# Kernel tuning notes

Measured on AMD Instinct MI355X. Metric: run time of the kernel, lower is better.

## Reference

```python
import jax, jax.numpy as jnp
import numpy as np

N_NODES = 50000
D_FEAT = 128
HIDDEN = 256
CLASSES = 40
N_EDGES = 800000


def setup_inputs() -> dict:
    key = jax.random.key(0)
    ks = jax.random.split(key, 8)
    x = jax.random.normal(ks[0], (N_NODES, D_FEAT), dtype=jnp.float32)
    edge_index = jax.random.randint(ks[1], (2, N_EDGES), 0, N_NODES, dtype=jnp.int64)
    s1 = 1.0 / np.sqrt(D_FEAT)
    s2 = 1.0 / np.sqrt(HIDDEN)
    # PyG SAGEConv: lin_l (applied to aggregated neighbors, has bias), lin_r (root, no bias)
    Wl1 = jax.random.uniform(ks[2], (HIDDEN, D_FEAT), jnp.float32, -s1, s1)
    bl1 = jnp.zeros((HIDDEN,), jnp.float32)
    Wr1 = jax.random.uniform(ks[3], (HIDDEN, D_FEAT), jnp.float32, -s1, s1)
    Wl2 = jax.random.uniform(ks[4], (CLASSES, HIDDEN), jnp.float32, -s2, s2)
    bl2 = jnp.zeros((CLASSES,), jnp.float32)
    Wr2 = jax.random.uniform(ks[5], (CLASSES, HIDDEN), jnp.float32, -s2, s2)
    return {"x": x, "edge_index": edge_index, "Wl1": Wl1, "bl1": bl1, "Wr1": Wr1,
            "Wl2": Wl2, "bl2": bl2, "Wr2": Wr2}


def _mean_aggregate(x, src, dst, n_nodes):
    # gather source features along edges, scatter-mean into destinations
    summed = jax.ops.segment_sum(x[src], dst, num_segments=n_nodes)  # [N, d]
    counts = jax.ops.segment_sum(jnp.ones((src.shape[0],), x.dtype), dst,
                                 num_segments=n_nodes)
    return summed / jnp.maximum(counts, 1.0)[:, None]


def _sage_conv(x, src, dst, Wl, bl, Wr):
    agg = _mean_aggregate(x, src, dst, x.shape[0])
    return agg @ Wl.T + bl + x @ Wr.T


def reference(x, edge_index, Wl1, bl1, Wr1, Wl2, bl2, Wr2):
    src, dst = edge_index[0], edge_index[1]
    h = _sage_conv(x, src, dst, Wl1, bl1, Wr1)
    h = jax.nn.relu(h)
    # F.dropout(training=self.training): eval-mode inference -> identity
    h = _sage_conv(h, src, dst, Wl2, bl2, Wr2)
    return jax.nn.log_softmax(h, axis=1)
```

## Files before the change

### kernel.cpp

```cpp
#include <hip/hip_runtime.h>
#include <hip/hip_bf16.h>
#include <math.h>

#define N_NODES 50000
#define D_FEAT  128
#define HIDDEN  256
#define CLASSES 40
#define N_EDGES 800000
#define R2S 48
#define HLS 264
#define ALS 136
#define NTILES 3125
#define GRID_L 512
#define NBUCK 196
#define BCAP  5120
#define BA_BLOCKS 784
#define WCVT_BLOCKS 336

typedef unsigned int  u32;
typedef unsigned short u16;
typedef __attribute__((ext_vector_type(8))) short short8;
typedef __attribute__((ext_vector_type(4))) float floatx4;

__device__ __forceinline__ float bf_lo(u32 w) { union { u32 i; float f; } u; u.i = w << 16; return u.f; }
__device__ __forceinline__ float bf_hi(u32 w) { union { u32 i; float f; } u; u.i = w & 0xffff0000u; return u.f; }
__device__ __forceinline__ float bf1(u16 h)   { union { u32 i; float f; } u; u.i = ((u32)h) << 16; return u.f; }
__device__ __forceinline__ u16 f2bf(float f) {
  union { float f; u32 i; } u; u.f = f; u32 i = u.i;
  return (u16)((i + 0x7fffu + ((i >> 16) & 1u)) >> 16);
}
__device__ __forceinline__ u32 packbf(float a, float b) { return (u32)f2bf(a) | ((u32)f2bf(b) << 16); }

__device__ __forceinline__ bool edges_are_i64(const void* eraw) {
  const long long* p = (const long long*)eraw;
  bool ok = true;
  #pragma unroll
  for (int i = 0; i < 8; i++) {
    long long v = p[(size_t)i * 100003];
    ok = ok && (v >= 0) && (v < N_NODES);
  }
  return ok;
}

__global__ __launch_bounds__(256) void cvt_x_kernel(
    const float* __restrict__ x, u16* __restrict__ xb, int* __restrict__ bcur) {
  if (blockIdx.x < 6250) {
    int i = (blockIdx.x * 256 + threadIdx.x) * 4;
    float4 v = *(const float4*)(x + i);
    u32* o = (u32*)(xb + i);
    o[0] = packbf(v.x, v.y);
    o[1] = packbf(v.z, v.w);
  } else {
    if (threadIdx.x < NBUCK) bcur[threadIdx.x] = 0;
  }
}

__global__ __launch_bounds__(256) void bucketA_kernel(
    const void* __restrict__ eraw, int* __restrict__ bcur, u32* __restrict__ bbuf,
    const float* __restrict__ Wl1, const float* __restrict__ Wr1,
    const float* __restrict__ Wl2, const float* __restrict__ Wr2,
    u16* __restrict__ wb) {
  if (blockIdx.x >= BA_BLOCKS) {
    int i = (blockIdx.x - BA_BLOCKS) * 256 + threadIdx.x;
    if (i < 32768)      wb[i] = f2bf(Wl1[i]);
    else if (i < 65536) wb[i] = f2bf(Wr1[i - 32768]);
    else if (i < 75776) wb[i] = f2bf(Wl2[i - 65536]);
    else if (i < 86016) wb[i] = f2bf(Wr2[i - 75776]);
    return;
  }
  __shared__ int hist[NBUCK], base[NBUCK], loc[NBUCK];
  const bool i64f = edges_are_i64(eraw);
  const int t = threadIdx.x;
  for (int i = t; i < NBUCK; i += 256) { hist[i] = 0; loc[i] = 0; }
  __syncthreads();

  int sreg[4], dreg[4];
  const int e0 = blockIdx.x * 1024;
  #pragma unroll
  for (int j = 0; j < 4; j++) {
    int e = e0 + j * 256 + t;
    int ss = 0, dd = -1;
    if (e < N_EDGES) {
      if (i64f) {
        const long long* p = (const long long*)eraw;
        ss = (int)p[e]; dd = (int)p[N_EDGES + e];
      } else {
        const int* p = (const int*)eraw;
        ss = p[e]; dd = p[N_EDGES + e];
      }
      if ((u32)ss >= N_NODES || (u32)dd >= N_NODES) dd = -1;
    }
    sreg[j] = ss; dreg[j] = dd;
    if (dd >= 0) atomicAdd(&hist[dd >> 8], 1);
  }
  __syncthreads();
  for (int i = t; i < NBUCK; i += 256)
    base[i] = atomicAdd(&bcur[i], hist[i]);
  __syncthreads();
  #pragma unroll
  for (int j = 0; j < 4; j++) {
    int dd = dreg[j];
    if (dd >= 0) {
      int bk = dd >> 8;
      int pos = base[bk] + atomicAdd(&loc[bk], 1);
      if (pos < BCAP)
        bbuf[(size_t)bk * BCAP + pos] = (u32)sreg[j] | ((u32)(dd & 255) << 16);
    }
  }
}

__global__ __launch_bounds__(256) void bucketBC_kernel(
    const u32* __restrict__ bbuf, const int* __restrict__ bcur,
    int* __restrict__ offsets, int* __restrict__ csr) {
  __shared__ int cnt[256];
  __shared__ int lds[256];
  const int t = threadIdx.x;
  const int b = blockIdx.x;
  int c196 = (t < NBUCK) ? min(bcur[t], BCAP) : 0;
  lds[t] = c196;
  __syncthreads();
  #pragma unroll
  for (int d = 1; d < 256; d <<= 1) {
    int v = (t >= d) ? lds[t - d] : 0;
    __syncthreads();
    lds[t] += v;
    __syncthreads();
  }
  const int btop = (b > 0) ? lds[b - 1] : 0;
  if (b == NBUCK - 1 && t == 0) offsets[N_NODES] = lds[NBUCK - 1];
  cnt[t] = 0;
  __syncthreads();
  const int n = min(bcur[b], BCAP);
  for (int i = t; i < n; i += 256) {
    u32 e = bbuf[(size_t)b * BCAP + i];
    atomicAdd(&cnt[(e >> 16) & 255], 1);
  }
  __syncthreads();
  int c = cnt[t];
  lds[t] = c;
  __syncthreads();
  #pragma unroll
  for (int d = 1; d < 256; d <<= 1) {
    int v = (t >= d) ? lds[t - d] : 0;
    __syncthreads();
    lds[t] += v;
    __syncthreads();
  }
  const int node = b * 256 + t;
  const int off = lds[t] - c + btop;
  if (node < N_NODES) offsets[node] = off;
  cnt[t] = off;
  __syncthreads();
  for (int i = t; i < n; i += 256) {
    u32 e = bbuf[(size_t)b * BCAP + i];
    int dl = (e >> 16) & 255;
    int pos = atomicAdd(&cnt[dl], 1);
    csr[pos] = (int)(e & 0xFFFFu);
  }
}

__global__ __launch_bounds__(256) void gather1_kernel(
    const u16* __restrict__ xb, const int* __restrict__ offsets,
    const int* __restrict__ csr_src, u16* __restrict__ agg1) {
  const int node = blockIdx.x * 4 + (threadIdx.x >> 6);
  const int lane = threadIdx.x & 63;
  int b = offsets[node], e = offsets[node + 1];
  float a0 = 0.f, a1 = 0.f, b0 = 0.f, b1 = 0.f;
  float c0 = 0.f, c1 = 0.f, d0 = 0.f, d1 = 0.f;
  float e0 = 0.f, e1 = 0.f, f0 = 0.f, f1 = 0.f;
  float g0 = 0.f, g1 = 0.f, h0 = 0.f, h1 = 0.f;
  int i = b;
  for (; i + 8 <= e; i += 8) {
    int s0 = csr_src[i],     s1 = csr_src[i + 1], s2 = csr_src[i + 2], s3 = csr_src[i + 3];
    int s4 = csr_src[i + 4], s5 = csr_src[i + 5], s6 = csr_src[i + 6], s7 = csr_src[i + 7];
    u32 w0 = ((const u32*)(xb + (size_t)s0 * D_FEAT))[lane];
    u32 w1 = ((const u32*)(xb + (size_t)s1 * D_FEAT))[lane];
    u32 w2 = ((const u32*)(xb + (size_t)s2 * D_FEAT))[lane];
    u32 w3 = ((const u32*)(xb + (size_t)s3 * D_FEAT))[lane];
    u32 w4 = ((const u32*)(xb + (size_t)s4 * D_FEAT))[lane];
    u32 w5 = ((const u32*)(xb + (size_t)s5 * D_FEAT))[lane];
    u32 w6 = ((const u32*)(xb + (size_t)s6 * D_FEAT))[lane];
    u32 w7 = ((const u32*)(xb + (size_t)s7 * D_FEAT))[lane];
    a0 += bf_lo(w0); a1 += bf_hi(w0);
    b0 += bf_lo(w1); b1 += bf_hi(w1);
    c0 += bf_lo(w2); c1 += bf_hi(w2);
    d0 += bf_lo(w3); d1 += bf_hi(w3);
    e0 += bf_lo(w4); e1 += bf_hi(w4);
    f0 += bf_lo(w5); f1 += bf_hi(w5);
    g0 += bf_lo(w6); g1 += bf_hi(w6);
    h0 += bf_lo(w7); h1 += bf_hi(w7);
  }
  for (; i < e; i++) {
    int s = csr_src[i];
    u32 w = ((const u32*)(xb + (size_t)s * D_FEAT))[lane];
    a0 += bf_lo(w); a1 += bf_hi(w);
  }
  float s0 = ((a0 + b0) + (c0 + d0)) + ((e0 + f0) + (g0 + h0));
  float s1 = ((a1 + b1) + (c1 + d1)) + ((e1 + f1) + (g1 + h1));
  float inv = 1.0f / (float)max(e - b, 1);
  ((u32*)(agg1 + (size_t)node * D_FEAT))[lane] = packbf(s0 * inv, s1 * inv);
}

__global__ __launch_bounds__(256, 2) void layer_kernel(
    const u16* __restrict__ agg1, const u16* __restrict__ xb,
    const u16* __restrict__ Wl1b, const u16* __restrict__ Wr1b,
    const float* __restrict__ bl1,
    const u16* __restrict__ Wl2b, const u16* __restrict__ Wr2b,
    const float* __restrict__ bl2,
    u16* __restrict__ p2a, u16* __restrict__ p2c, float* __restrict__ r2f) {
  __shared__ u16 h_lds[16 * HLS];
  __shared__ u16 a_lds[16 * ALS];
  __shared__ u16 x_lds[16 * ALS];
  const int lane = threadIdx.x & 63;
  const int wave = threadIdx.x >> 6;
  const int n15  = lane & 15;
  const int quad = lane >> 4;
  const int ko   = quad * 8;
  const int colbase = wave * 64;
  const int srow = (wave << 2) + quad;
  const int scol = n15 * 8;

  short8 Bf[8][4];
  #pragma unroll
  for (int s = 0; s < 8; s++) {
    const u16* W = (s < 4) ? Wl1b : Wr1b;
    const int kk = (s & 3) * 32;
    #pragma unroll
    for (int t = 0; t < 4; t++)
      Bf[s][t] = *(const short8*)(W + (size_t)(colbase + t * 16 + n15) * D_FEAT + ko + kk);
  }

  const int  c0   = wave;
  const bool isR0 = (c0 >= 3);
  const int  tc0  = c0 - (isR0 ? 3 : 0);
  const int  wr0  = min(tc0 * 16 + n15, CLASSES - 1);
  const u16* Wc0  = (isR0 ? Wr2b : Wl2b) + (size_t)wr0 * HIDDEN + ko;
  const bool has1 = (wave < 2);
  const int  tc1  = wave + 1;
  const int  wr1  = min(tc1 * 16 + n15, CLASSES - 1);
  const u16* Wc1  = Wr2b + (size_t)wr1 * HIDDEN + ko;

  const float bias0 = bl2[min(tc0 * 16 + n15, CLASSES - 1)];
  const float bias1 = bl2[min(tc1 * 16 + n15, CLASSES - 1)];

  for (int tile = blockIdx.x; tile < NTILES; tile += GRID_L) {
    const int m0 = tile * 16;
    {
      const size_t g = (size_t)(m0 + srow) * D_FEAT + scol;
      *(short8*)(a_lds + srow * ALS + scol) = *(const short8*)(agg1 + g);
      *(short8*)(x_lds + srow * ALS + scol) = *(const short8*)(xb + g);
    }
    __syncthreads();
    {
      floatx4 acc[4];
      #pragma unroll
      for (int t = 0; t < 4; t++) acc[t] = floatx4{0.f, 0.f, 0.f, 0.f};

      short8 a[4];
      #pragma unroll
      for (int s = 0; s < 4; s++) a[s] = *(const short8*)(a_lds + n15 * ALS + ko + s * 32);
      #pragma unroll
      for (int s = 0; s < 4; s++)
        #pragma unroll
        for (int t = 0; t < 4; t++)
          acc[t] = __builtin_amdgcn_mfma_f32_16x16x32_bf16(a[s], Bf[s][t], acc[t], 0, 0, 0);
      #pragma unroll
      for (int s = 0; s < 4; s++) a[s] = *(const short8*)(x_lds + n15 * ALS + ko + s * 32);
      #pragma unroll
      for (int s = 0; s < 4; s++)
        #pragma unroll
        for (int t = 0; t < 4; t++)
          acc[t] = __builtin_amdgcn_mfma_f32_16x16x32_bf16(a[s], Bf[4 + s][t], acc[t], 0, 0, 0);

      #pragma unroll
      for (int t = 0; t < 4; t++) {
        int col = colbase + t * 16 + n15;
        float bias = bl1[col];
        #pragma unroll
        for (int r = 0; r < 4; r++) {
          float v = acc[t][r] + bias;
          v = v > 0.f ? v : 0.f;
          h_lds[(quad * 4 + r) * HLS + col] = f2bf(v);
        }
      }
    }
    __syncthreads();
    {
      floatx4 acc0 = floatx4{0.f, 0.f, 0.f, 0.f};
      floatx4 acc1 = floatx4{0.f, 0.f, 0.f, 0.f};
      #pragma unroll
      for (int s = 0; s < 8; s++) {
        short8 a2 = *(const short8*)(&h_lds[n15 * HLS + s * 32 + ko]);
        acc0 = __builtin_amdgcn_mfma_f32_16x16x32_bf16(a2, *(const short8*)(Wc0 + s * 32), acc0, 0, 0, 0);
        if (has1)
          acc1 = __builtin_amdgcn_mfma_f32_16x16x32_bf16(a2, *(const short8*)(Wc1 + s * 32), acc1, 0, 0, 0);
      }
      {
        int col = tc0 * 16 + n15;
        #pragma unroll
        for (int r = 0; r < 4; r++) {
          int row = m0 + quad * 4 + r;
          if (isR0) {
            r2f[(size_t)row * R2S + col] = acc0[r] + bias0;
          } else if (col < 32) {
            p2a[(size_t)row * 32 + col] = f2bf(acc0[r]);
          } else if (col < CLASSES) {
            p2c[(size_t)row * 8 + (col - 32)] = f2bf(acc0[r]);
          }
        }
      }
      if (has1) {
        int col = tc1 * 16 + n15;
        #pragma unroll
        for (int r = 0; r < 4; r++) {
          int row = m0 + quad * 4 + r;
          r2f[(size_t)row * R2S + col] = acc1[r] + bias1;
        }
      }
    }
    __syncthreads();
  }
}

__global__ __launch_bounds__(256) void final_kernel(
    const u16* __restrict__ p2a, const u16* __restrict__ p2c,
    const float* __restrict__ r2f,
    const int* __restrict__ offsets, const int* __restrict__ csr_src,
    float* __restrict__ out) {
  const int node = blockIdx.x * 4 + (threadIdx.x >> 6);
  const int lane = threadIdx.x & 63;
  const u16* gb = (lane < 32) ? (p2a + lane) : (p2c + min(lane - 32, 7));
  const int  gs = (lane < 32) ? 32 : 8;
  int b = offsets[node], e = offsets[node + 1];
  float s[16];
  #pragma unroll
  for (int j = 0; j < 16; j++) s[j] = 0.f;
  int i = b;
  for (; i + 16 <= e; i += 16) {
    int c[16];
    #pragma unroll
    for (int j = 0; j < 16; j++) c[j] = csr_src[i + j];
    #pragma unroll
    for (int j = 0; j < 16; j++) s[j] += bf1(gb[(size_t)c[j] * gs]);
  }
  for (; i + 8 <= e; i += 8) {
    int c[8];
    #pragma unroll
    for (int j = 0; j < 8; j++) c[j] = csr_src[i + j];
    #pragma unroll
    for (int j = 0; j < 8; j++) s[j] += bf1(gb[(size_t)c[j] * gs]);
  }
  for (; i < e; i++) {
    int sc = csr_src[i];
    s[0] += bf1(gb[(size_t)sc * gs]);
  }
  float sum4[4];
  #pragma unroll
  for (int j = 0; j < 4; j++)
    sum4[j] = (s[j] + s[j + 4]) + (s[j + 8] + s[j + 12]);
  float ssum = (sum4[0] + sum4[1]) + (sum4[2] + sum4[3]);
  float inv = 1.0f / (float)max(e - b, 1);
  const bool act = (lane < CLASSES);
  float v = act ? (ssum * inv + r2f[(size_t)node * R2S + lane]) : -INFINITY;
  float mx = v;
  #pragma unroll
  for (int d = 1; d < 64; d <<= 1) mx = fmaxf(mx, __shfl_xor(mx, d, 64));
  float ex = act ? expf(v - mx) : 0.f;
  float sum = ex;
  #pragma unroll
  for (int d = 1; d < 64; d <<= 1) sum += __shfl_xor(sum, d, 64);
  float l = mx + logf(sum);
  if (act) out[(size_t)node * CLASSES + lane] = v - l;
}

extern "C" void kernel_launch(void* const* d_in, const int* in_sizes, int n_in,
                              void* d_out, int out_size, void* d_ws, size_t ws_size,
                              hipStream_t stream) {
  const float* x   = (const float*)d_in[0];
  const void*  ei  = d_in[1];
  const float* Wl1 = (const float*)d_in[2];
  const float* bl1 = (const float*)d_in[3];
  const float* Wr1 = (const float*)d_in[4];
  const float* Wl2 = (const float*)d_in[5];
  const float* bl2 = (const float*)d_in[6];
  const float* Wr2 = (const float*)d_in[7];

  char* ws = (char*)d_ws;
  size_t off = 0;
  int* csr       = (int*)(ws + off); off += (size_t)N_EDGES * 4;
  int* offsets   = (int*)(ws + off); off += 204800;
  int* bcur      = (int*)(ws + off); off += 1024;
  u32* bbuf      = (u32*)(ws + off); off += (size_t)NBUCK * BCAP * 4;
  u16* wb        = (u16*)(ws + off); off += 172288;
  u16* xb        = (u16*)(ws + off); off += (size_t)N_NODES * D_FEAT * 2;
  u16* agg1      = (u16*)(ws + off); off += (size_t)N_NODES * D_FEAT * 2;
  u16* p2a       = (u16*)(ws + off); off += (size_t)N_NODES * 32 * 2;
  u16* p2c       = (u16*)(ws + off); off += (size_t)N_NODES * 8 * 2;
  float* r2f     = (float*)(ws + off); off += (size_t)N_NODES * R2S * 4;

  u16* Wl1b = wb;
  u16* Wr1b = wb + 32768;
  u16* Wl2b = wb + 65536;
  u16* Wr2b = wb + 75776;

  cvt_x_kernel<<<6251, 256, 0, stream>>>(x, xb, bcur);
  bucketA_kernel<<<BA_BLOCKS + WCVT_BLOCKS, 256, 0, stream>>>(
      ei, bcur, bbuf, Wl1, Wr1, Wl2, Wr2, wb);
  bucketBC_kernel<<<NBUCK, 256, 0, stream>>>(bbuf, bcur, offsets, csr);
  gather1_kernel<<<N_NODES / 4, 256, 0, stream>>>(xb, offsets, csr, agg1);
  layer_kernel<<<GRID_L, 256, 0, stream>>>(agg1, xb, Wl1b, Wr1b, bl1,
                                           Wl2b, Wr2b, bl2, p2a, p2c, r2f);
  final_kernel<<<N_NODES / 4, 256, 0, stream>>>(p2a, p2c, r2f, offsets, csr, (float*)d_out);
}
```

Baseline: 225.4 us.

## Fuse preprocessing, CSR build and first aggregation into one cooperative kernel

Merges the x/weight conversion, the two bucket-sort CSR stages and the layer-1 neighbour gather into a single cooperative kernel of 1024 persistent blocks, with grid-wide syncs between phases. This removes three kernel launches and their launch gaps. In exchange each phase now runs on a fixed grid with grid-stride loops, and grid.sync adds barrier cost. Only 196 or 784 blocks do useful work in the bucket phases while the rest sit idle at the barrier.

```diff
diff --git a/kernel.cpp b/kernel.cpp
--- a/kernel.cpp
+++ b/kernel.cpp
@@ -1,5 +1,6 @@
 #include <hip/hip_runtime.h>
 #include <hip/hip_bf16.h>
+#include <hip/hip_cooperative_groups.h>
 #include <math.h>
 
 #define N_NODES 50000
@@ -15,7 +16,10 @@
 #define NBUCK 196
 #define BCAP  5120
 #define BA_BLOCKS 784
-#define WCVT_BLOCKS 336
+#define GRID_M 1024
+#define CVT_CHUNKS 6587
+
+namespace cg = cooperative_groups;
 
 typedef unsigned int  u32;
 typedef unsigned short u16;
@@ -42,163 +46,166 @@
   return ok;
 }
 
-__global__ __launch_bounds__(256) void cvt_x_kernel(
-    const float* __restrict__ x, u16* __restrict__ xb, int* __restrict__ bcur) {
-  if (blockIdx.x < 6250) {
-    int i = (blockIdx.x * 256 + threadIdx.x) * 4;
-    float4 v = *(const float4*)(x + i);
-    u32* o = (u32*)(xb + i);
-    o[0] = packbf(v.x, v.y);
-    o[1] = packbf(v.z, v.w);
-  } else {
-    if (threadIdx.x < NBUCK) bcur[threadIdx.x] = 0;
-  }
-}
-
-__global__ __launch_bounds__(256) void bucketA_kernel(
-    const void* __restrict__ eraw, int* __restrict__ bcur, u32* __restrict__ bbuf,
+__global__ __launch_bounds__(256, 4) void mega1_kernel(
+    const float* __restrict__ x,
     const float* __restrict__ Wl1, const float* __restrict__ Wr1,
     const float* __restrict__ Wl2, const float* __restrict__ Wr2,
-    u16* __restrict__ wb) {
-  if (blockIdx.x >= BA_BLOCKS) {
-    int i = (blockIdx.x - BA_BLOCKS) * 256 + threadIdx.x;
-    if (i < 32768)      wb[i] = f2bf(Wl1[i]);
-    else if (i < 65536) wb[i] = f2bf(Wr1[i - 32768]);
-    else if (i < 75776) wb[i] = f2bf(Wl2[i - 65536]);
-    else if (i < 86016) wb[i] = f2bf(Wr2[i - 75776]);
-    return;
-  }
+    u16* __restrict__ xb, u16* __restrict__ wb,
+    const void* __restrict__ eraw, int* __restrict__ bcur,
+    u32* __restrict__ bbuf, int* __restrict__ offsets, int* __restrict__ csr,
+    u16* __restrict__ agg1) {
+  cg::grid_group grid = cg::this_grid();
   __shared__ int hist[NBUCK], base[NBUCK], loc[NBUCK];
-  const bool i64f = edges_are_i64(eraw);
-  const int t = threadIdx.x;
-  for (int i = t; i < NBUCK; i += 256) { hist[i] = 0; loc[i] = 0; }
-  __syncthreads();
-
-  int sreg[4], dreg[4];
-  const int e0 = blockIdx.x * 1024;
-  #pragma unroll
-  for (int j = 0; j < 4; j++) {
-    int e = e0 + j * 256 + t;
-    int ss = 0, dd = -1;
-    if (e < N_EDGES) {
-      if (i64f) {
-        const long long* p = (const long long*)eraw;
-        ss = (int)p[e]; dd = (int)p[N_EDGES + e];
-      } else {
-        const int* p = (const int*)eraw;
-        ss = p[e]; dd = p[N_EDGES + e];
-      }
-      if ((u32)ss >= N_NODES || (u32)dd >= N_NODES) dd = -1;
-    }
-    sreg[j] = ss; dreg[j] = dd;
-    if (dd >= 0) atomicAdd(&hist[dd >> 8], 1);
-  }
-  __syncthreads();
-  for (int i = t; i < NBUCK; i += 256)
-    base[i] = atomicAdd(&bcur[i], hist[i]);
-  __syncthreads();
-  #pragma unroll
-  for (int j = 0; j < 4; j++) {
-    int dd = dreg[j];
-    if (dd >= 0) {
-      int bk = dd >> 8;
-      int pos = base[bk] + atomicAdd(&loc[bk], 1);
-      if (pos < BCAP)
-        bbuf[(size_t)bk * BCAP + pos] = (u32)sreg[j] | ((u32)(dd & 255) << 16);
-    }
-  }
-}
-
-__global__ __launch_bounds__(256) void bucketBC_kernel(
-    const u32* __restrict__ bbuf, const int* __restrict__ bcur,
-    int* __restrict__ offsets, int* __restrict__ csr) {
-  __shared__ int cnt[256];
-  __shared__ int lds[256];
+  __shared__ int cnt[256], lds[256];
   const int t = threadIdx.x;
   const int b = blockIdx.x;
-  int c196 = (t < NBUCK) ? min(bcur[t], BCAP) : 0;
-  lds[t] = c196;
-  __syncthreads();
-  #pragma unroll
-  for (int d = 1; d < 256; d <<= 1) {
-    int v = (t >= d) ? lds[t - d] : 0;
-    __syncthreads();
-    lds[t] += v;
-    __syncthreads();
-  }
-  const int btop = (b > 0) ? lds[b - 1] : 0;
-  if (b == NBUCK - 1 && t == 0) offsets[N_NODES] = lds[NBUCK - 1];
-  cnt[t] = 0;
-  __syncthreads();
-  const int n = min(bcur[b], BCAP);
-  for (int i = t; i < n; i += 256) {
-    u32 e = bbuf[(size_t)b * BCAP + i];
-    atomicAdd(&cnt[(e >> 16) & 255], 1);
-  }
-  __syncthreads();
-  int c = cnt[t];
-  lds[t] = c;
-  __syncthreads();
-  #pragma unroll
-  for (int d = 1; d < 256; d <<= 1) {
-    int v = (t >= d) ? lds[t - d] : 0;
-    __syncthreads();
-    lds[t] += v;
-    __syncthreads();
-  }
-  const int node = b * 256 + t;
-  const int off = lds[t] - c + btop;
-  if (node < N_NODES) offsets[node] = off;
-  cnt[t] = off;
-  __syncthreads();
-  for (int i = t; i < n; i += 256) {
-    u32 e = bbuf[(size_t)b * BCAP + i];
-    int dl = (e >> 16) & 255;
-    int pos = atomicAdd(&cnt[dl], 1);
-    csr[pos] = (int)(e & 0xFFFFu);
-  }
-}
-
-__global__ __launch_bounds__(256) void gather1_kernel(
-    const u16* __restrict__ xb, const int* __restrict__ offsets,
-    const int* __restrict__ csr_src, u16* __restrict__ agg1) {
-  const int node = blockIdx.x * 4 + (threadIdx.x >> 6);
-  const int lane = threadIdx.x & 63;
-  int b = offsets[node], e = offsets[node + 1];
-  float a0 = 0.f, a1 = 0.f, b0 = 0.f, b1 = 0.f;
-  float c0 = 0.f, c1 = 0.f, d0 = 0.f, d1 = 0.f;
-  float e0 = 0.f, e1 = 0.f, f0 = 0.f, f1 = 0.f;
-  float g0 = 0.f, g1 = 0.f, h0 = 0.f, h1 = 0.f;
-  int i = b;
-  for (; i + 8 <= e; i += 8) {
-    int s0 = csr_src[i],     s1 = csr_src[i + 1], s2 = csr_src[i + 2], s3 = csr_src[i + 3];
-    int s4 = csr_src[i + 4], s5 = csr_src[i + 5], s6 = csr_src[i + 6], s7 = csr_src[i + 7];
-    u32 w0 = ((const u32*)(xb + (size_t)s0 * D_FEAT))[lane];
-    u32 w1 = ((const u32*)(xb + (size_t)s1 * D_FEAT))[lane];
-    u32 w2 = ((const u32*)(xb + (size_t)s2 * D_FEAT))[lane];
-    u32 w3 = ((const u32*)(xb + (size_t)s3 * D_FEAT))[lane];
-    u32 w4 = ((const u32*)(xb + (size_t)s4 * D_FEAT))[lane];
-    u32 w5 = ((const u32*)(xb + (size_t)s5 * D_FEAT))[lane];
-    u32 w6 = ((const u32*)(xb + (size_t)s6 * D_FEAT))[lane];
-    u32 w7 = ((const u32*)(xb + (size_t)s7 * D_FEAT))[lane];
-    a0 += bf_lo(w0); a1 += bf_hi(w0);
-    b0 += bf_lo(w1); b1 += bf_hi(w1);
-    c0 += bf_lo(w2); c1 += bf_hi(w2);
-    d0 += bf_lo(w3); d1 += bf_hi(w3);
-    e0 += bf_lo(w4); e1 += bf_hi(w4);
-    f0 += bf_lo(w5); f1 += bf_hi(w5);
-    g0 += bf_lo(w6); g1 += bf_hi(w6);
-    h0 += bf_lo(w7); h1 += bf_hi(w7);
-  }
-  for (; i < e; i++) {
-    int s = csr_src[i];
-    u32 w = ((const u32*)(xb + (size_t)s * D_FEAT))[lane];
-    a0 += bf_lo(w); a1 += bf_hi(w);
-  }
-  float s0 = ((a0 + b0) + (c0 + d0)) + ((e0 + f0) + (g0 + h0));
-  float s1 = ((a1 + b1) + (c1 + d1)) + ((e1 + f1) + (g1 + h1));
-  float inv = 1.0f / (float)max(e - b, 1);
-  ((u32*)(agg1 + (size_t)node * D_FEAT))[lane] = packbf(s0 * inv, s1 * inv);
+
+  for (int blk = b; blk < CVT_CHUNKS; blk += GRID_M) {
+    if (blk < 6250) {
+      int i = (blk * 256 + t) * 4;
+      float4 v = *(const float4*)(x + i);
+      u32* o = (u32*)(xb + i);
+      o[0] = packbf(v.x, v.y);
+      o[1] = packbf(v.z, v.w);
+    } else if (blk < 6586) {
+      int i = (blk - 6250) * 256 + t;
+      if (i < 32768)      wb[i] = f2bf(Wl1[i]);
+      else if (i < 65536) wb[i] = f2bf(Wr1[i - 32768]);
+      else if (i < 75776) wb[i] = f2bf(Wl2[i - 65536]);
+      else if (i < 86016) wb[i] = f2bf(Wr2[i - 75776]);
+    } else {
+      if (t < NBUCK) bcur[t] = 0;
+    }
+  }
+  grid.sync();
+
+  if (b < BA_BLOCKS) {
+    const bool i64f = edges_are_i64(eraw);
+    for (int i = t; i < NBUCK; i += 256) { hist[i] = 0; loc[i] = 0; }
+    __syncthreads();
+    int sreg[4], dreg[4];
+    const int e0 = b * 1024;
+    #pragma unroll
+    for (int j = 0; j < 4; j++) {
+      int e = e0 + j * 256 + t;
+      int ss = 0, dd = -1;
+      if (e < N_EDGES) {
+        if (i64f) {
+          const long long* p = (const long long*)eraw;
+          ss = (int)p[e]; dd = (int)p[N_EDGES + e];
+        } else {
+          const int* p = (const int*)eraw;
+          ss = p[e]; dd = p[N_EDGES + e];
+        }
+        if ((u32)ss >= N_NODES || (u32)dd >= N_NODES) dd = -1;
+      }
+      sreg[j] = ss; dreg[j] = dd;
+      if (dd >= 0) atomicAdd(&hist[dd >> 8], 1);
+    }
+    __syncthreads();
+    for (int i = t; i < NBUCK; i += 256)
+      base[i] = atomicAdd(&bcur[i], hist[i]);
+    __syncthreads();
+    #pragma unroll
+    for (int j = 0; j < 4; j++) {
+      int dd = dreg[j];
+      if (dd >= 0) {
+        int bk = dd >> 8;
+        int pos = base[bk] + atomicAdd(&loc[bk], 1);
+        if (pos < BCAP)
+          bbuf[(size_t)bk * BCAP + pos] = (u32)sreg[j] | ((u32)(dd & 255) << 16);
+      }
+    }
+  }
+  grid.sync();
+
+  if (b < NBUCK) {
+    int c196 = (t < NBUCK) ? min(bcur[t], BCAP) : 0;
+    lds[t] = c196;
+    __syncthreads();
+    #pragma unroll
+    for (int d = 1; d < 256; d <<= 1) {
+      int v = (t >= d) ? lds[t - d] : 0;
+      __syncthreads();
+      lds[t] += v;
+      __syncthreads();
+    }
+    const int btop = (b > 0) ? lds[b - 1] : 0;
+    if (b == NBUCK - 1 && t == 0) offsets[N_NODES] = lds[NBUCK - 1];
+    cnt[t] = 0;
+    __syncthreads();
+    const int n = min(bcur[b], BCAP);
+    for (int i = t; i < n; i += 256) {
+      u32 e = bbuf[(size_t)b * BCAP + i];
+      atomicAdd(&cnt[(e >> 16) & 255], 1);
+    }
+    __syncthreads();
+    int c = cnt[t];
+    lds[t] = c;
+    __syncthreads();
+    #pragma unroll
+    for (int d = 1; d < 256; d <<= 1) {
+      int v = (t >= d) ? lds[t - d] : 0;
+      __syncthreads();
+      lds[t] += v;
+      __syncthreads();
+    }
+    const int node = b * 256 + t;
+    const int off = lds[t] - c + btop;
+    if (node < N_NODES) offsets[node] = off;
+    cnt[t] = off;
+    __syncthreads();
+    for (int i = t; i < n; i += 256) {
+      u32 e = bbuf[(size_t)b * BCAP + i];
+      int dl = (e >> 16) & 255;
+      int pos = atomicAdd(&cnt[dl], 1);
+      csr[pos] = (int)(e & 0xFFFFu);
+    }
+  }
+  grid.sync();
+
+  {
+    const int wave = t >> 6;
+    const int lane = t & 63;
+    for (int g = b; g < N_NODES / 4; g += GRID_M) {
+      const int node = g * 4 + wave;
+      int bo = offsets[node], e = offsets[node + 1];
+      float a0 = 0.f, a1 = 0.f, b0 = 0.f, b1 = 0.f;
+      float c0 = 0.f, c1 = 0.f, d0 = 0.f, d1 = 0.f;
+      float e0 = 0.f, e1 = 0.f, f0 = 0.f, f1 = 0.f;
+      float g0 = 0.f, g1 = 0.f, h0 = 0.f, h1 = 0.f;
+      int i = bo;
+      for (; i + 8 <= e; i += 8) {
+        int s0 = csr[i],     s1 = csr[i + 1], s2 = csr[i + 2], s3 = csr[i + 3];
+        int s4 = csr[i + 4], s5 = csr[i + 5], s6 = csr[i + 6], s7 = csr[i + 7];
+        u32 w0 = ((const u32*)(xb + (size_t)s0 * D_FEAT))[lane];
+        u32 w1 = ((const u32*)(xb + (size_t)s1 * D_FEAT))[lane];
+        u32 w2 = ((const u32*)(xb + (size_t)s2 * D_FEAT))[lane];
+        u32 w3 = ((const u32*)(xb + (size_t)s3 * D_FEAT))[lane];
+        u32 w4 = ((const u32*)(xb + (size_t)s4 * D_FEAT))[lane];
+        u32 w5 = ((const u32*)(xb + (size_t)s5 * D_FEAT))[lane];
+        u32 w6 = ((const u32*)(xb + (size_t)s6 * D_FEAT))[lane];
+        u32 w7 = ((const u32*)(xb + (size_t)s7 * D_FEAT))[lane];
+        a0 += bf_lo(w0); a1 += bf_hi(w0);
+        b0 += bf_lo(w1); b1 += bf_hi(w1);
+        c0 += bf_lo(w2); c1 += bf_hi(w2);
+        d0 += bf_lo(w3); d1 += bf_hi(w3);
+        e0 += bf_lo(w4); e1 += bf_hi(w4);
+        f0 += bf_lo(w5); f1 += bf_hi(w5);
+        g0 += bf_lo(w6); g1 += bf_hi(w6);
+        h0 += bf_lo(w7); h1 += bf_hi(w7);
+      }
+      for (; i < e; i++) {
+        int s = csr[i];
+        u32 w = ((const u32*)(xb + (size_t)s * D_FEAT))[lane];
+        a0 += bf_lo(w); a1 += bf_hi(w);
+      }
+      float s0 = ((a0 + b0) + (c0 + d0)) + ((e0 + f0) + (g0 + h0));
+      float s1 = ((a1 + b1) + (c1 + d1)) + ((e1 + f1) + (g1 + h1));
+      float inv = 1.0f / (float)max(e - bo, 1);
+      ((u32*)(agg1 + (size_t)node * D_FEAT))[lane] = packbf(s0 * inv, s1 * inv);
+    }
+  }
 }
 
 __global__ __launch_bounds__(256, 2) void layer_kernel(
@@ -403,11 +410,10 @@
   u16* Wl2b = wb + 65536;
   u16* Wr2b = wb + 75776;
 
-  cvt_x_kernel<<<6251, 256, 0, stream>>>(x, xb, bcur);
-  bucketA_kernel<<<BA_BLOCKS + WCVT_BLOCKS, 256, 0, stream>>>(
-      ei, bcur, bbuf, Wl1, Wr1, Wl2, Wr2, wb);
-  bucketBC_kernel<<<NBUCK, 256, 0, stream>>>(bbuf, bcur, offsets, csr);
-  gather1_kernel<<<N_NODES / 4, 256, 0, stream>>>(xb, offsets, csr, agg1);
+  void* args[] = { (void*)&x, (void*)&Wl1, (void*)&Wr1, (void*)&Wl2, (void*)&Wr2,
+                   (void*)&xb, (void*)&wb, (void*)&ei, (void*)&bcur, (void*)&bbuf,
+                   (void*)&offsets, (void*)&csr, (void*)&agg1 };
+  hipLaunchCooperativeKernel((void*)mega1_kernel, dim3(GRID_M), dim3(256), args, 0, stream);
   layer_kernel<<<GRID_L, 256, 0, stream>>>(agg1, xb, Wl1b, Wr1b, bl1,
                                            Wl2b, Wr2b, bl2, p2a, p2c, r2f);
   final_kernel<<<N_NODES / 4, 256, 0, stream>>>(p2a, p2c, r2f, offsets, csr, (float*)d_out);
```

Measured after the change: 551.7 us. +144.7%, slower.

## Merge p2 buffers into padded 64-wide rows and gather two edges per wave

Applied to the files above, without the earlier changes.

The two layer-2 projection buffers (32-wide and 8-wide) are replaced by one bf16 buffer with a 64-element row stride. The final gather then reads packed u32 pairs, so each half-wave handles a different edge and the two halves are combined with shuffles. This is meant to cut per-edge load instructions and make the gather accesses coalesced. The cost is a larger intermediate buffer whose padding columns are never read, plus extra shuffle work at the end.

```diff
diff --git a/kernel.cpp b/kernel.cpp
--- a/kernel.cpp
+++ b/kernel.cpp
@@ -7,6 +7,7 @@
 #define HIDDEN  256
 #define CLASSES 40
 #define N_EDGES 800000
+#define P2S 64
 #define R2S 48
 #define HLS 264
 #define ALS 136
@@ -207,7 +208,7 @@
     const float* __restrict__ bl1,
     const u16* __restrict__ Wl2b, const u16* __restrict__ Wr2b,
     const float* __restrict__ bl2,
-    u16* __restrict__ p2a, u16* __restrict__ p2c, float* __restrict__ r2f) {
+    u16* __restrict__ p2b, float* __restrict__ r2f) {
   __shared__ u16 h_lds[16 * HLS];
   __shared__ u16 a_lds[16 * ALS];
   __shared__ u16 x_lds[16 * ALS];
@@ -300,13 +301,8 @@
         #pragma unroll
         for (int r = 0; r < 4; r++) {
           int row = m0 + quad * 4 + r;
-          if (isR0) {
-            r2f[(size_t)row * R2S + col] = acc0[r] + bias0;
-          } else if (col < 32) {
-            p2a[(size_t)row * 32 + col] = f2bf(acc0[r]);
-          } else if (col < CLASSES) {
-            p2c[(size_t)row * 8 + (col - 32)] = f2bf(acc0[r]);
-          }
+          if (isR0) r2f[(size_t)row * R2S + col] = acc0[r] + bias0;
+          else      p2b[(size_t)row * P2S + col] = f2bf(acc0[r]);
         }
       }
       if (has1) {
@@ -323,42 +319,42 @@
 }
 
 __global__ __launch_bounds__(256) void final_kernel(
-    const u16* __restrict__ p2a, const u16* __restrict__ p2c,
-    const float* __restrict__ r2f,
+    const u16* __restrict__ p2b, const float* __restrict__ r2f,
     const int* __restrict__ offsets, const int* __restrict__ csr_src,
     float* __restrict__ out) {
-  const int node = blockIdx.x * 4 + (threadIdx.x >> 6);
-  const int lane = threadIdx.x & 63;
-  const u16* gb = (lane < 32) ? (p2a + lane) : (p2c + min(lane - 32, 7));
-  const int  gs = (lane < 32) ? 32 : 8;
+  const int node  = blockIdx.x * 4 + (threadIdx.x >> 6);
+  const int lane  = threadIdx.x & 63;
+  const int eslot = lane >> 5;
+  const int k     = lane & 31;
+  const u32* p2w  = (const u32*)p2b;
   int b = offsets[node], e = offsets[node + 1];
-  float s[16];
-  #pragma unroll
-  for (int j = 0; j < 16; j++) s[j] = 0.f;
+  float slo = 0.f, shi = 0.f;
   int i = b;
   for (; i + 16 <= e; i += 16) {
-    int c[16];
-    #pragma unroll
-    for (int j = 0; j < 16; j++) c[j] = csr_src[i + j];
-    #pragma unroll
-    for (int j = 0; j < 16; j++) s[j] += bf1(gb[(size_t)c[j] * gs]);
-  }
-  for (; i + 8 <= e; i += 8) {
     int c[8];
     #pragma unroll
-    for (int j = 0; j < 8; j++) c[j] = csr_src[i + j];
+    for (int j = 0; j < 8; j++) c[j] = csr_src[i + 2 * j + eslot];
+    u32 w[8];
     #pragma unroll
-    for (int j = 0; j < 8; j++) s[j] += bf1(gb[(size_t)c[j] * gs]);
-  }
-  for (; i < e; i++) {
-    int sc = csr_src[i];
-    s[0] += bf1(gb[(size_t)sc * gs]);
-  }
-  float sum4[4];
-  #pragma unroll
-  for (int j = 0; j < 4; j++)
-    sum4[j] = (s[j] + s[j + 4]) + (s[j + 8] + s[j + 12]);
-  float ssum = (sum4[0] + sum4[1]) + (sum4[2] + sum4[3]);
+    for (int j = 0; j < 8; j++) w[j] = p2w[((u32)c[j] << 5) + k];
+    #pragma unroll
+    for (int j = 0; j < 8; j++) { slo += bf_lo(w[j]); shi += bf_hi(w[j]); }
+  }
+  for (; i + 2 <= e; i += 2) {
+    int c = csr_src[i + eslot];
+    u32 w = p2w[((u32)c << 5) + k];
+    slo += bf_lo(w); shi += bf_hi(w);
+  }
+  if (i < e && eslot == 0) {
+    int c = csr_src[i];
+    u32 w = p2w[((u32)c << 5) + k];
+    slo += bf_lo(w); shi += bf_hi(w);
+  }
+  slo += __shfl_xor(slo, 32, 64);
+  shi += __shfl_xor(shi, 32, 64);
+  float vlo = __shfl(slo, lane >> 1, 64);
+  float vhi = __shfl(shi, lane >> 1, 64);
+  float ssum = (lane & 1) ? vhi : vlo;
   float inv = 1.0f / (float)max(e - b, 1);
   const bool act = (lane < CLASSES);
   float v = act ? (ssum * inv + r2f[(size_t)node * R2S + lane]) : -INFINITY;
@@ -394,8 +390,7 @@
   u16* wb        = (u16*)(ws + off); off += 172288;
   u16* xb        = (u16*)(ws + off); off += (size_t)N_NODES * D_FEAT * 2;
   u16* agg1      = (u16*)(ws + off); off += (size_t)N_NODES * D_FEAT * 2;
-  u16* p2a       = (u16*)(ws + off); off += (size_t)N_NODES * 32 * 2;
-  u16* p2c       = (u16*)(ws + off); off += (size_t)N_NODES * 8 * 2;
+  u16* p2b       = (u16*)(ws + off); off += (size_t)N_NODES * P2S * 2;
   float* r2f     = (float*)(ws + off); off += (size_t)N_NODES * R2S * 4;
 
   u16* Wl1b = wb;
@@ -409,6 +404,6 @@
   bucketBC_kernel<<<NBUCK, 256, 0, stream>>>(bbuf, bcur, offsets, csr);
   gather1_kernel<<<N_NODES / 4, 256, 0, stream>>>(xb, offsets, csr, agg1);
   layer_kernel<<<GRID_L, 256, 0, stream>>>(agg1, xb, Wl1b, Wr1b, bl1,
-                                           Wl2b, Wr2b, bl2, p2a, p2c, r2f);
-  final_kernel<<<N_NODES / 4, 256, 0, stream>>>(p2a, p2c, r2f, offsets, csr, (float*)d_out);
-}
+                                           Wl2b, Wr2b, bl2, p2b, r2f);
+  final_kernel<<<N_NODES / 4, 256, 0, stream>>>(p2b, r2f, offsets, csr, (float*)d_out);
+}
```

Result: no change. 221.6 us (-1.7%).
